# Performance work log

Measured on AMD Instinct MI355X. Metric: run time of the kernel, lower is better.

## Reference

```python
import jax, jax.numpy as jnp
import numpy as np

EPS = 1e-6
C = 0.01  # global curvature from init_kwargs


def mobius_add(x, y, c):
    # x, y broadcastable [..., d]
    x2 = jnp.sum(x * x, axis=-1, keepdims=True)
    y2 = jnp.sum(y * y, axis=-1, keepdims=True)
    xy = jnp.sum(x * y, axis=-1, keepdims=True)
    num = (1 + 2 * c * xy + c * y2) * x + (1 - c * x2) * y
    den = 1 + 2 * c * xy + (c ** 2) * x2 * y2
    return num / (den + EPS)


def log_map_zero(x, c):
    sqrt_c = jnp.sqrt(c)
    norm = jnp.maximum(jnp.linalg.norm(x, axis=-1, keepdims=True), EPS)
    arg = jnp.minimum(sqrt_c * norm, 1.0 - 1e-5)
    return jnp.arctanh(arg) * x / (sqrt_c * norm)


def exp_map_zero(v, c):
    sqrt_c = jnp.sqrt(c)
    norm = jnp.maximum(jnp.linalg.norm(v, axis=-1, keepdims=True), EPS)
    return jnp.tanh(sqrt_c * norm) * v / (sqrt_c * norm)


def setup_inputs() -> dict:
    key = jax.random.key(0)
    k1, k2, k3, k4, k5, k6, k7 = jax.random.split(key, 7)
    num_entities, d = 20000, 256
    num_rel2 = 512  # num_relations * 2
    B = 1024
    # Poincare-ball embeddings: keep norms well inside radius 1/sqrt(c)=10
    entity_embedding = 0.05 * jax.random.normal(k1, (num_entities, d), dtype=jnp.float32)
    # relation embeddings live in tangent space
    rel_embedding = 0.05 * jax.random.normal(k2, (num_rel2, d), dtype=jnp.float32)
    s = jax.random.randint(k3, (B,), 0, num_entities)
    r = jax.random.randint(k4, (B,), 0, num_rel2)
    o = jax.random.randint(k5, (B,), 0, num_entities)
    triplets = jnp.stack([s, r, o], axis=1).astype(jnp.int64)
    xav = float(np.sqrt(6.0 / (d + d)))
    W_s = jax.random.uniform(k6, (d, d), dtype=jnp.float32, minval=-xav, maxval=xav)
    W_o = jax.random.uniform(k7, (d, d), dtype=jnp.float32, minval=-xav, maxval=xav)
    rel_bias = jnp.zeros((num_rel2,), dtype=jnp.float32)
    return {"entity_embedding": entity_embedding, "rel_embedding": rel_embedding,
            "triplets": triplets, "W_s": W_s, "W_o": W_o, "rel_bias": rel_bias}


def reference(entity_embedding, rel_embedding, triplets, W_s, W_o, rel_bias):
    c = C
    s_emb = entity_embedding[triplets[:, 0]]  # (B, d)
    o_emb = entity_embedding[triplets[:, 2]]  # (B, d)
    # tangent-space linear transforms (MuRP-style), dropout=0 -> identity
    s_tan = log_map_zero(s_emb, c) @ W_s
    o_tan = log_map_zero(o_emb, c) @ W_o
    s_h = exp_map_zero(s_tan, c)
    o_h = exp_map_zero(o_tan, c)
    # Mobius difference query q = (-h_s) (+)_c h_o
    query = mobius_add(-s_h, o_h, c)  # (B, d)
    # relation embeddings mapped from tangent space onto the ball
    rel_h = exp_map_zero(rel_embedding, c)  # (N, d)
    # proxy distance score: -||(-q) (+)_c r||^2 + bias, fully vectorized (B, N, d)
    diff = mobius_add(-query[:, None, :], rel_h[None, :, :], c)
    dist_sq = jnp.sum(diff * diff, axis=-1)  # (B, N)
    scores = -dist_sq + rel_bias[None, :]
    return scores
```

## Files before the change

kernel.cpp:

```cpp
#include <hip/hip_runtime.h>
#include <math.h>

#define EPSF 1e-6f
#define CCF  0.01f
#define SQRT_C 0.1f

typedef __attribute__((ext_vector_type(8))) short bf16x8;
typedef __attribute__((ext_vector_type(4))) float f32x4;

__device__ __forceinline__ float wred(float v) {
#pragma unroll
    for (int o = 32; o > 0; o >>= 1) v += __shfl_xor(v, o, 64);
    return v;
}
__device__ __forceinline__ unsigned f2bf1(float x) {
    unsigned u = __builtin_bit_cast(unsigned, x);
    return (u + 0x7FFFu + ((u >> 16) & 1u)) >> 16;
}
__device__ __forceinline__ uint2 pack4(float4 v) {
    uint2 r;
    r.x = f2bf1(v.x) | (f2bf1(v.y) << 16);
    r.y = f2bf1(v.z) | (f2bf1(v.w) << 16);
    return r;
}

__global__ __launch_bounds__(256) void k1(const float* __restrict__ E,
                                          const int* __restrict__ trip,
                                          const float* __restrict__ rel,
                                          const float* __restrict__ Ws,
                                          const float* __restrict__ Wo,
                                          unsigned short* __restrict__ xs,
                                          unsigned short* __restrict__ relbf,
                                          float* __restrict__ y2,
                                          unsigned short* __restrict__ WT) {
    __shared__ float tile[64][65];
    int blk = blockIdx.x;
    int t = threadIdx.x, w = t >> 6, lane = t & 63;
    if (blk < 512) {
        int z = blk * 4 + w;
        int b = z & 1023;
        int col = (z >> 10) ? 2 : 0;
        int idx = trip[b * 3 + col];
        idx = max(0, min(idx, 19999));
        float4 v = *(const float4*)(E + (size_t)idx * 256 + lane * 4);
        float ss = v.x * v.x;
        ss = fmaf(v.y, v.y, ss);
        ss = fmaf(v.z, v.z, ss);
        ss = fmaf(v.w, v.w, ss);
        ss = wred(ss);
        float n = fmaxf(sqrtf(ss), EPSF);
        float arg = fminf(SQRT_C * n, 1.f - 1e-5f);
        float s = atanhf(arg) / (SQRT_C * n);
        v.x *= s; v.y *= s; v.z *= s; v.w *= s;
        *(uint2*)(xs + (size_t)z * 256 + lane * 4) = pack4(v);
    } else if (blk < 528) {
#pragma unroll
        for (int rr = 0; rr < 8; ++rr) {
            int r = (blk - 512) * 32 + rr * 4 + w;
            float4 v = *(const float4*)(rel + (size_t)r * 256 + lane * 4);
            float ss = v.x * v.x;
            ss = fmaf(v.y, v.y, ss);
            ss = fmaf(v.z, v.z, ss);
            ss = fmaf(v.w, v.w, ss);
            ss = wred(ss);
            float n = fmaxf(sqrtf(ss), EPSF);
            float s = tanhf(SQRT_C * n) / (SQRT_C * n);
            v.x *= s; v.y *= s; v.z *= s; v.w *= s;
            *(uint2*)(relbf + (size_t)r * 256 + lane * 4) = pack4(v);
            if (lane == 0) y2[r] = s * s * ss;
        }
    } else {
        int blk2 = blk - 528;
        int mat = blk2 >> 4;
        int tl = blk2 & 15;
        int k0 = (tl >> 2) * 64, n0 = (tl & 3) * 64;
        const float* __restrict__ W = mat ? Wo : Ws;
#pragma unroll 4
        for (int p = 0; p < 16; ++p) {
            int i = p * 4 + w;
            tile[i][lane] = W[(size_t)(k0 + i) * 256 + n0 + lane];
        }
        __syncthreads();
#pragma unroll 4
        for (int p = 0; p < 16; ++p) {
            int n = p * 4 + w;
            WT[(size_t)mat * 65536 + (size_t)(n0 + n) * 256 + k0 + lane] =
                (unsigned short)f2bf1(tile[lane][n]);
        }
    }
}

__global__ __launch_bounds__(256) void k2(const unsigned short* __restrict__ xs,
                                          const unsigned short* __restrict__ WT,
                                          float* __restrict__ T) {
    __shared__ unsigned short Al[32 * 256];
    __shared__ unsigned short Bl[64 * 256];
    int bid = blockIdx.x;
    int M0 = (bid >> 2) * 32, N0 = (bid & 3) * 64;
    int mat = (M0 >= 1024);
    int t = threadIdx.x, w = t >> 6, lane = t & 63;
    int row16 = lane & 15, g = lane >> 4;
    char* Ab = (char*)Al;
    char* Bb = (char*)Bl;
#pragma unroll
    for (int i = 0; i < 4; ++i) {
        int L = i * 256 + t, r = L >> 5, c = L & 31;
        bf16x8 v = *(const bf16x8*)(xs + (size_t)(M0 + r) * 256 + c * 8);
        *(bf16x8*)(Ab + r * 512 + ((c * 16) ^ ((r & 7) << 4))) = v;
    }
#pragma unroll
    for (int i = 0; i < 8; ++i) {
        int L = i * 256 + t, r = L >> 5, c = L & 31;
        bf16x8 v = *(const bf16x8*)(WT + (size_t)mat * 65536 + (size_t)(N0 + r) * 256 + c * 8);
        *(bf16x8*)(Bb + r * 512 + ((c * 16) ^ ((r & 7) << 4))) = v;
    }
    __syncthreads();
    int wm = (w >> 1) * 16, wn = (w & 1) * 32;
    f32x4 acc0 = {0.f, 0.f, 0.f, 0.f};
    f32x4 acc1 = {0.f, 0.f, 0.f, 0.f};
    int mr = wm + row16, n0r = wn + row16, n1r = wn + 16 + row16;
#pragma unroll
    for (int kt = 0; kt < 8; ++kt) {
        bf16x8 a  = *(const bf16x8*)(Ab + mr * 512 + ((kt * 64 + g * 16) ^ ((mr & 7) << 4)));
        bf16x8 b0 = *(const bf16x8*)(Bb + n0r * 512 + ((kt * 64 + g * 16) ^ ((n0r & 7) << 4)));
        bf16x8 b1 = *(const bf16x8*)(Bb + n1r * 512 + ((kt * 64 + g * 16) ^ ((n1r & 7) << 4)));
        acc0 = __builtin_amdgcn_mfma_f32_16x16x32_bf16(a, b0, acc0, 0, 0, 0);
        acc1 = __builtin_amdgcn_mfma_f32_16x16x32_bf16(a, b1, acc1, 0, 0, 0);
    }
#pragma unroll
    for (int i = 0; i < 4; ++i) {
        int m = M0 + wm + g * 4 + i;
        T[(size_t)m * 256 + N0 + wn + row16]      = acc0[i];
        T[(size_t)m * 256 + N0 + wn + 16 + row16] = acc1[i];
    }
}

__global__ __launch_bounds__(512) void k3(const float* __restrict__ T,
                                          unsigned short* __restrict__ qbf,
                                          float* __restrict__ q2) {
    int t = threadIdx.x, w = t >> 6, lane = t & 63;
    int b = blockIdx.x * 8 + w;
    float4 sv = *(const float4*)(T + (size_t)b * 256 + lane * 4);
    float4 ov = *(const float4*)(T + (size_t)(1024 + b) * 256 + lane * 4);
    float sss = sv.x * sv.x, sso = ov.x * ov.x, sdot = sv.x * ov.x;
    sss = fmaf(sv.y, sv.y, sss); sso = fmaf(ov.y, ov.y, sso); sdot = fmaf(sv.y, ov.y, sdot);
    sss = fmaf(sv.z, sv.z, sss); sso = fmaf(ov.z, ov.z, sso); sdot = fmaf(sv.z, ov.z, sdot);
    sss = fmaf(sv.w, sv.w, sss); sso = fmaf(ov.w, ov.w, sso); sdot = fmaf(sv.w, ov.w, sdot);
    sss = wred(sss); sso = wred(sso); sdot = wred(sdot);
    float ns = fmaxf(sqrtf(sss), EPSF);
    float no = fmaxf(sqrtf(sso), EPSF);
    float scs = tanhf(SQRT_C * ns) / (SQRT_C * ns);
    float sco = tanhf(SQRT_C * no) / (SQRT_C * no);
    float x2 = scs * scs * sss;
    float yy2 = sco * sco * sso;
    float xy = -scs * sco * sdot;
    float a1 = 1.f + 2.f * CCF * xy + CCF * yy2;
    float b1 = 1.f - CCF * x2;
    float den = 1.f + 2.f * CCF * xy + CCF * CCF * x2 * yy2 + EPSF;
    float rden = 1.f / den;
    float4 qv;
    qv.x = (a1 * (-scs * sv.x) + b1 * (sco * ov.x)) * rden;
    qv.y = (a1 * (-scs * sv.y) + b1 * (sco * ov.y)) * rden;
    qv.z = (a1 * (-scs * sv.z) + b1 * (sco * ov.z)) * rden;
    qv.w = (a1 * (-scs * sv.w) + b1 * (sco * ov.w)) * rden;
    float qq = qv.x * qv.x;
    qq = fmaf(qv.y, qv.y, qq);
    qq = fmaf(qv.z, qv.z, qq);
    qq = fmaf(qv.w, qv.w, qq);
    qq = wred(qq);
    *(uint2*)(qbf + (size_t)b * 256 + lane * 4) = pack4(qv);
    if (lane == 0) q2[b] = qq;
}

__global__ __launch_bounds__(256) void k4(const unsigned short* __restrict__ qbf,
                                          const unsigned short* __restrict__ relbf,
                                          const float* __restrict__ q2,
                                          const float* __restrict__ y2,
                                          const float* __restrict__ rbias,
                                          float* __restrict__ out) {
    __shared__ unsigned short Al[32 * 256];
    __shared__ unsigned short Bl[64 * 256];
    __shared__ float q2l[32], y2l[64], rbl[64];
    int bid = blockIdx.x;
    int M0 = (bid >> 3) * 32, N0 = (bid & 7) * 64;
    int t = threadIdx.x, w = t >> 6, lane = t & 63;
    int row16 = lane & 15, g = lane >> 4;
    char* Ab = (char*)Al;
    char* Bb = (char*)Bl;
#pragma unroll
    for (int i = 0; i < 4; ++i) {
        int L = i * 256 + t, r = L >> 5, c = L & 31;
        bf16x8 v = *(const bf16x8*)(qbf + (size_t)(M0 + r) * 256 + c * 8);
        *(bf16x8*)(Ab + r * 512 + ((c * 16) ^ ((r & 7) << 4))) = v;
    }
#pragma unroll
    for (int i = 0; i < 8; ++i) {
        int L = i * 256 + t, r = L >> 5, c = L & 31;
        bf16x8 v = *(const bf16x8*)(relbf + (size_t)(N0 + r) * 256 + c * 8);
        *(bf16x8*)(Bb + r * 512 + ((c * 16) ^ ((r & 7) << 4))) = v;
    }
    if (t < 32) q2l[t] = q2[M0 + t];
    else if (t < 96) y2l[t - 32] = y2[N0 + t - 32];
    else if (t < 160) rbl[t - 96] = rbias[N0 + t - 96];
    __syncthreads();
    int wm = (w >> 1) * 16, wn = (w & 1) * 32;
    f32x4 acc0 = {0.f, 0.f, 0.f, 0.f};
    f32x4 acc1 = {0.f, 0.f, 0.f, 0.f};
    int mr = wm + row16, n0r = wn + row16, n1r = wn + 16 + row16;
#pragma unroll
    for (int kt = 0; kt < 8; ++kt) {
        bf16x8 a  = *(const bf16x8*)(Ab + mr * 512 + ((kt * 64 + g * 16) ^ ((mr & 7) << 4)));
        bf16x8 b0 = *(const bf16x8*)(Bb + n0r * 512 + ((kt * 64 + g * 16) ^ ((n0r & 7) << 4)));
        bf16x8 b1 = *(const bf16x8*)(Bb + n1r * 512 + ((kt * 64 + g * 16) ^ ((n1r & 7) << 4)));
        acc0 = __builtin_amdgcn_mfma_f32_16x16x32_bf16(a, b0, acc0, 0, 0, 0);
        acc1 = __builtin_amdgcn_mfma_f32_16x16x32_bf16(a, b1, acc1, 0, 0, 0);
    }
#pragma unroll
    for (int tt = 0; tt < 2; ++tt) {
        int rloc = wn + tt * 16 + row16;
        int r = N0 + rloc;
        f32x4 a = tt ? acc1 : acc0;
        float y2r = y2l[rloc];
        float rb = rbl[rloc];
#pragma unroll
        for (int i = 0; i < 4; ++i) {
            int mloc = wm + g * 4 + i;
            float xy = -a[i];
            float x2 = q2l[mloc];
            float a1 = 1.f + 2.f * CCF * xy + CCF * y2r;
            float b1 = 1.f - CCF * x2;
            float den = 1.f + 2.f * CCF * xy + CCF * CCF * x2 * y2r + EPSF;
            float num2 = a1 * a1 * x2 + 2.f * a1 * b1 * xy + b1 * b1 * y2r;
            out[(size_t)(M0 + mloc) * 512 + r] = -(num2 / (den * den)) + rb;
        }
    }
}

extern "C" void kernel_launch(void* const* d_in, const int* in_sizes, int n_in,
                              void* d_out, int out_size, void* d_ws, size_t ws_size,
                              hipStream_t stream) {
    const float* E = (const float*)d_in[0];
    const float* rel = (const float*)d_in[1];
    const int* trip = (const int*)d_in[2];
    const float* Ws = (const float*)d_in[3];
    const float* Wo = (const float*)d_in[4];
    const float* rbias = (const float*)d_in[5];
    float* out = (float*)d_out;

    char* p = (char*)d_ws;
    unsigned short* xs    = (unsigned short*)p;  p += (size_t)2048 * 256 * 2;
    float*          T     = (float*)p;           p += (size_t)2048 * 256 * 4;
    unsigned short* qbf   = (unsigned short*)p;  p += (size_t)1024 * 256 * 2;
    float*          q2    = (float*)p;           p += 4096;
    unsigned short* relbf = (unsigned short*)p;  p += (size_t)512 * 256 * 2;
    float*          y2    = (float*)p;           p += 2048;
    unsigned short* WT    = (unsigned short*)p;  p += (size_t)2 * 256 * 256 * 2;

    k1<<<560, 256, 0, stream>>>(E, trip, rel, Ws, Wo, xs, relbf, y2, WT);
    k2<<<256, 256, 0, stream>>>(xs, WT, T);
    k3<<<128, 512, 0, stream>>>(T, qbf, q2);
    k4<<<256, 256, 0, stream>>>(qbf, relbf, q2, y2, rbias, out);
}
```

Measured before the change: 22.60 us.

## Fuse tangent-space GEMM and Mobius query kernels via shared-memory tile

Merges the projection GEMM kernel and the per-row Mobius query kernel into one kernel. Each block computes 16 subject rows and the matching 16 object rows across all 256 output columns, keeps the result in LDS, and then derives q and its squared norm there. This removes one launch and the global round trip of the fp32 intermediate T. In exchange there are only 64 blocks, so fewer CUs are busy, and each block reloads the full W matrices in four chunks with a barrier around each load.

```diff
diff --git a/kernel.cpp b/kernel.cpp
--- a/kernel.cpp
+++ b/kernel.cpp
@@ -90,86 +90,89 @@
     }
 }
 
-__global__ __launch_bounds__(256) void k2(const unsigned short* __restrict__ xs,
-                                          const unsigned short* __restrict__ WT,
-                                          float* __restrict__ T) {
+__global__ __launch_bounds__(512) void k23(const unsigned short* __restrict__ xs,
+                                           const unsigned short* __restrict__ WT,
+                                           unsigned short* __restrict__ qbf,
+                                           float* __restrict__ q2) {
     __shared__ unsigned short Al[32 * 256];
-    __shared__ unsigned short Bl[64 * 256];
-    int bid = blockIdx.x;
-    int M0 = (bid >> 2) * 32, N0 = (bid & 3) * 64;
-    int mat = (M0 >= 1024);
+    __shared__ unsigned short Bl[128 * 256];
+    __shared__ float T[32][256];
+    int P0 = blockIdx.x * 16;
     int t = threadIdx.x, w = t >> 6, lane = t & 63;
     int row16 = lane & 15, g = lane >> 4;
     char* Ab = (char*)Al;
     char* Bb = (char*)Bl;
-#pragma unroll
-    for (int i = 0; i < 4; ++i) {
-        int L = i * 256 + t, r = L >> 5, c = L & 31;
-        bf16x8 v = *(const bf16x8*)(xs + (size_t)(M0 + r) * 256 + c * 8);
+
+#pragma unroll
+    for (int i = 0; i < 2; ++i) {
+        int L = i * 512 + t, r = L >> 5, c = L & 31;
+        int zr = (r < 16) ? (P0 + r) : (1024 + P0 + r - 16);
+        bf16x8 v = *(const bf16x8*)(xs + (size_t)zr * 256 + c * 8);
         *(bf16x8*)(Ab + r * 512 + ((c * 16) ^ ((r & 7) << 4))) = v;
     }
-#pragma unroll
-    for (int i = 0; i < 8; ++i) {
-        int L = i * 256 + t, r = L >> 5, c = L & 31;
-        bf16x8 v = *(const bf16x8*)(WT + (size_t)mat * 65536 + (size_t)(N0 + r) * 256 + c * 8);
-        *(bf16x8*)(Bb + r * 512 + ((c * 16) ^ ((r & 7) << 4))) = v;
+
+    int mat = w >> 2;
+    int mr = mat * 16 + row16;
+    int nsub = (w & 3) * 16;
+#pragma unroll
+    for (int nc = 0; nc < 4; ++nc) {
+        __syncthreads();
+#pragma unroll
+        for (int i = 0; i < 8; ++i) {
+            int L = i * 512 + t, r = L >> 5, c = L & 31;
+            int m2 = r >> 6, n = nc * 64 + (r & 63);
+            bf16x8 v = *(const bf16x8*)(WT + (size_t)m2 * 65536 + (size_t)n * 256 + c * 8);
+            *(bf16x8*)(Bb + r * 512 + ((c * 16) ^ ((r & 7) << 4))) = v;
+        }
+        __syncthreads();
+        int nr = mat * 64 + nsub + row16;
+        f32x4 acc = {0.f, 0.f, 0.f, 0.f};
+#pragma unroll
+        for (int kt = 0; kt < 8; ++kt) {
+            bf16x8 a = *(const bf16x8*)(Ab + mr * 512 + ((kt * 64 + g * 16) ^ ((mr & 7) << 4)));
+            bf16x8 b = *(const bf16x8*)(Bb + nr * 512 + ((kt * 64 + g * 16) ^ ((nr & 7) << 4)));
+            acc = __builtin_amdgcn_mfma_f32_16x16x32_bf16(a, b, acc, 0, 0, 0);
+        }
+#pragma unroll
+        for (int i = 0; i < 4; ++i)
+            T[mat * 16 + g * 4 + i][nc * 64 + nsub + row16] = acc[i];
     }
     __syncthreads();
-    int wm = (w >> 1) * 16, wn = (w & 1) * 32;
-    f32x4 acc0 = {0.f, 0.f, 0.f, 0.f};
-    f32x4 acc1 = {0.f, 0.f, 0.f, 0.f};
-    int mr = wm + row16, n0r = wn + row16, n1r = wn + 16 + row16;
-#pragma unroll
-    for (int kt = 0; kt < 8; ++kt) {
-        bf16x8 a  = *(const bf16x8*)(Ab + mr * 512 + ((kt * 64 + g * 16) ^ ((mr & 7) << 4)));
-        bf16x8 b0 = *(const bf16x8*)(Bb + n0r * 512 + ((kt * 64 + g * 16) ^ ((n0r & 7) << 4)));
-        bf16x8 b1 = *(const bf16x8*)(Bb + n1r * 512 + ((kt * 64 + g * 16) ^ ((n1r & 7) << 4)));
-        acc0 = __builtin_amdgcn_mfma_f32_16x16x32_bf16(a, b0, acc0, 0, 0, 0);
-        acc1 = __builtin_amdgcn_mfma_f32_16x16x32_bf16(a, b1, acc1, 0, 0, 0);
-    }
-#pragma unroll
-    for (int i = 0; i < 4; ++i) {
-        int m = M0 + wm + g * 4 + i;
-        T[(size_t)m * 256 + N0 + wn + row16]      = acc0[i];
-        T[(size_t)m * 256 + N0 + wn + 16 + row16] = acc1[i];
-    }
-}
-
-__global__ __launch_bounds__(512) void k3(const float* __restrict__ T,
-                                          unsigned short* __restrict__ qbf,
-                                          float* __restrict__ q2) {
-    int t = threadIdx.x, w = t >> 6, lane = t & 63;
-    int b = blockIdx.x * 8 + w;
-    float4 sv = *(const float4*)(T + (size_t)b * 256 + lane * 4);
-    float4 ov = *(const float4*)(T + (size_t)(1024 + b) * 256 + lane * 4);
-    float sss = sv.x * sv.x, sso = ov.x * ov.x, sdot = sv.x * ov.x;
-    sss = fmaf(sv.y, sv.y, sss); sso = fmaf(ov.y, ov.y, sso); sdot = fmaf(sv.y, ov.y, sdot);
-    sss = fmaf(sv.z, sv.z, sss); sso = fmaf(ov.z, ov.z, sso); sdot = fmaf(sv.z, ov.z, sdot);
-    sss = fmaf(sv.w, sv.w, sss); sso = fmaf(ov.w, ov.w, sso); sdot = fmaf(sv.w, ov.w, sdot);
-    sss = wred(sss); sso = wred(sso); sdot = wred(sdot);
-    float ns = fmaxf(sqrtf(sss), EPSF);
-    float no = fmaxf(sqrtf(sso), EPSF);
-    float scs = tanhf(SQRT_C * ns) / (SQRT_C * ns);
-    float sco = tanhf(SQRT_C * no) / (SQRT_C * no);
-    float x2 = scs * scs * sss;
-    float yy2 = sco * sco * sso;
-    float xy = -scs * sco * sdot;
-    float a1 = 1.f + 2.f * CCF * xy + CCF * yy2;
-    float b1 = 1.f - CCF * x2;
-    float den = 1.f + 2.f * CCF * xy + CCF * CCF * x2 * yy2 + EPSF;
-    float rden = 1.f / den;
-    float4 qv;
-    qv.x = (a1 * (-scs * sv.x) + b1 * (sco * ov.x)) * rden;
-    qv.y = (a1 * (-scs * sv.y) + b1 * (sco * ov.y)) * rden;
-    qv.z = (a1 * (-scs * sv.z) + b1 * (sco * ov.z)) * rden;
-    qv.w = (a1 * (-scs * sv.w) + b1 * (sco * ov.w)) * rden;
-    float qq = qv.x * qv.x;
-    qq = fmaf(qv.y, qv.y, qq);
-    qq = fmaf(qv.z, qv.z, qq);
-    qq = fmaf(qv.w, qv.w, qq);
-    qq = wred(qq);
-    *(uint2*)(qbf + (size_t)b * 256 + lane * 4) = pack4(qv);
-    if (lane == 0) q2[b] = qq;
+
+#pragma unroll
+    for (int j = 0; j < 2; ++j) {
+        int p = w * 2 + j;
+        float4 sv = *(const float4*)&T[p][lane * 4];
+        float4 ov = *(const float4*)&T[16 + p][lane * 4];
+        float sss = sv.x * sv.x, sso = ov.x * ov.x, sdot = sv.x * ov.x;
+        sss = fmaf(sv.y, sv.y, sss); sso = fmaf(ov.y, ov.y, sso); sdot = fmaf(sv.y, ov.y, sdot);
+        sss = fmaf(sv.z, sv.z, sss); sso = fmaf(ov.z, ov.z, sso); sdot = fmaf(sv.z, ov.z, sdot);
+        sss = fmaf(sv.w, sv.w, sss); sso = fmaf(ov.w, ov.w, sso); sdot = fmaf(sv.w, ov.w, sdot);
+        sss = wred(sss); sso = wred(sso); sdot = wred(sdot);
+        float ns = fmaxf(sqrtf(sss), EPSF);
+        float no = fmaxf(sqrtf(sso), EPSF);
+        float scs = tanhf(SQRT_C * ns) / (SQRT_C * ns);
+        float sco = tanhf(SQRT_C * no) / (SQRT_C * no);
+        float x2 = scs * scs * sss;
+        float yy2 = sco * sco * sso;
+        float xy = -scs * sco * sdot;
+        float a1 = 1.f + 2.f * CCF * xy + CCF * yy2;
+        float b1 = 1.f - CCF * x2;
+        float den = 1.f + 2.f * CCF * xy + CCF * CCF * x2 * yy2 + EPSF;
+        float rden = 1.f / den;
+        float4 qv;
+        qv.x = (a1 * (-scs * sv.x) + b1 * (sco * ov.x)) * rden;
+        qv.y = (a1 * (-scs * sv.y) + b1 * (sco * ov.y)) * rden;
+        qv.z = (a1 * (-scs * sv.z) + b1 * (sco * ov.z)) * rden;
+        qv.w = (a1 * (-scs * sv.w) + b1 * (sco * ov.w)) * rden;
+        float qq = qv.x * qv.x;
+        qq = fmaf(qv.y, qv.y, qq);
+        qq = fmaf(qv.z, qv.z, qq);
+        qq = fmaf(qv.w, qv.w, qq);
+        qq = wred(qq);
+        *(uint2*)(qbf + (size_t)(P0 + p) * 256 + lane * 4) = pack4(qv);
+        if (lane == 0) q2[P0 + p] = qq;
+    }
 }
 
 __global__ __launch_bounds__(256) void k4(const unsigned short* __restrict__ qbf,
@@ -249,7 +252,6 @@
 
     char* p = (char*)d_ws;
     unsigned short* xs    = (unsigned short*)p;  p += (size_t)2048 * 256 * 2;
-    float*          T     = (float*)p;           p += (size_t)2048 * 256 * 4;
     unsigned short* qbf   = (unsigned short*)p;  p += (size_t)1024 * 256 * 2;
     float*          q2    = (float*)p;           p += 4096;
     unsigned short* relbf = (unsigned short*)p;  p += (size_t)512 * 256 * 2;
@@ -257,7 +259,6 @@
     unsigned short* WT    = (unsigned short*)p;  p += (size_t)2 * 256 * 256 * 2;
 
     k1<<<560, 256, 0, stream>>>(E, trip, rel, Ws, Wo, xs, relbf, y2, WT);
-    k2<<<256, 256, 0, stream>>>(xs, WT, T);
-    k3<<<128, 512, 0, stream>>>(T, qbf, q2);
+    k23<<<64, 512, 0, stream>>>(xs, WT, qbf, q2);
     k4<<<256, 256, 0, stream>>>(qbf, relbf, q2, y2, rbias, out);
 }
```

After: 25.33 us. +12.0%, slower.
